# Kernel optimization log

Hardware: AMD Instinct MI355X
Metric: run time of the kernel (lower is better)

The kernel has to match this reference:

```python
import jax, jax.numpy as jnp
import numpy as np

N_NODES = 50000
N_EDGES = 800000
IN_CH = 128
HID = 128
OUT_CH = 10
N_GRAPHS = 64
BN_EPS = 1e-5


def _lin_init(k, fan_in, fan_out):
    k1, k2 = jax.random.split(k)
    s = 1.0 / np.sqrt(fan_in)
    W = jax.random.uniform(k1, (fan_in, fan_out), minval=-s, maxval=s, dtype=jnp.float32)
    b = jax.random.uniform(k2, (fan_out,), minval=-s, maxval=s, dtype=jnp.float32)
    return W, b


def setup_inputs() -> dict:
    key = jax.random.key(0)
    ks = jax.random.split(key, 12)
    x = jax.random.normal(ks[0], (N_NODES, IN_CH), dtype=jnp.float32)
    edge_index = jax.random.randint(ks[1], (2, N_EDGES), 0, N_NODES, dtype=jnp.int32)
    batch = jnp.sort(jax.random.randint(ks[2], (N_NODES,), 0, N_GRAPHS, dtype=jnp.int32))
    Wb0, bb0 = _lin_init(ks[3], IN_CH, HID)
    Wb1, bb1 = _lin_init(ks[4], HID, HID)
    Wa0, ba0 = _lin_init(ks[5], HID, HID)
    Wa1, ba1 = _lin_init(ks[6], HID, HID)
    Wa2, ba2 = _lin_init(ks[7], HID, HID)
    Wh0, bh0 = _lin_init(ks[8], HID, HID)
    Wh1, bh1 = _lin_init(ks[9], HID, HID)
    Wh2, bh2 = _lin_init(ks[10], HID, OUT_CH)
    ones = jnp.ones((HID,), jnp.float32)
    zeros = jnp.zeros((HID,), jnp.float32)
    return {
        'x': x, 'edge_index': edge_index, 'batch': batch, 'num_graphs': N_GRAPHS,
        'Wb0': Wb0, 'bb0': bb0, 'gb0': ones, 'betab0': zeros, 'Wb1': Wb1, 'bb1': bb1,
        'Wa0': Wa0, 'ba0': ba0, 'ga0': ones, 'bea0': zeros,
        'Wa1': Wa1, 'ba1': ba1, 'ga1': ones, 'bea1': zeros,
        'Wa2': Wa2, 'ba2': ba2,
        'Wh0': Wh0, 'bh0': bh0, 'Wh1': Wh1, 'bh1': bh1, 'Wh2': Wh2, 'bh2': bh2,
    }


def _gcn_edges(edge_index, n):
    # add self-loops, symmetric deg^{-1/2} normalization (PyG GCNConv default)
    loop = jnp.arange(n, dtype=edge_index.dtype)
    src = jnp.concatenate([edge_index[0], loop])
    dst = jnp.concatenate([edge_index[1], loop])
    deg = jax.ops.segment_sum(jnp.ones_like(dst, dtype=jnp.float32), dst, num_segments=n)
    dinv = jnp.where(deg > 0, jax.lax.rsqrt(deg), 0.0)
    return src, dst, dinv[src] * dinv[dst]


def _conv(h, W, b, src, dst, ew, n):
    hw = h @ W  # [N, F_out]
    agg = jax.ops.segment_sum(hw[src] * ew[:, None], dst, num_segments=n)
    return agg + b


def _bn(h, g, b):
    # BatchNorm1d with track_running_stats=False -> always batch statistics
    mean = jnp.mean(h, axis=0)
    var = jnp.var(h, axis=0)
    return g * (h - mean) * jax.lax.rsqrt(var + BN_EPS) + b


def _gelu(h):
    return jax.nn.gelu(h, approximate=False)


def reference(x, edge_index, batch, num_graphs,
              Wb0, bb0, gb0, betab0, Wb1, bb1,
              Wa0, ba0, ga0, bea0, Wa1, ba1, ga1, bea1, Wa2, ba2,
              Wh0, bh0, Wh1, bh1, Wh2, bh2):
    n = x.shape[0]
    src, dst, ew = _gcn_edges(edge_index, n)
    # GCN stack before (2 layers): conv -> bn -> gelu -> conv
    h = _conv(x, Wb0, bb0, src, dst, ew, n)
    h = _gelu(_bn(h, gb0, betab0))
    h = _conv(h, Wb1, bb1, src, dst, ew, n)
    # GCN stack after (3 layers)
    h = _conv(h, Wa0, ba0, src, dst, ew, n)
    h = _gelu(_bn(h, ga0, bea0))
    h = _conv(h, Wa1, ba1, src, dst, ew, n)
    h = _gelu(_bn(h, ga1, bea1))
    h = _conv(h, Wa2, ba2, src, dst, ew, n)
    # global mean pool per graph
    sums = jax.ops.segment_sum(h, batch, num_segments=num_graphs)
    cnt = jax.ops.segment_sum(jnp.ones((n,), jnp.float32), batch, num_segments=num_graphs)
    pooled = sums / jnp.maximum(cnt, 1.0)[:, None]
    # MLP head (dropout is identity in eval)
    y = _gelu(pooled @ Wh0 + bh0)
    y = _gelu(y @ Wh1 + bh1)
    return y @ Wh2 + bh2
```

## Files before the change

kernel.cpp:

```cpp
#include <hip/hip_runtime.h>
#include <math.h>

#define NN 50000
#define NE 800000
#define CH 128
#define NG 64
#define BN_EPS 1e-5f
#define POOL_CHUNK 64
#define BKT_SHIFT 9
#define NBKT ((NN + 511) >> 9)
#define PTILE 2048
#define NPART ((NE + PTILE - 1) / PTILE)
#define CAP 16384

typedef short bfrag8 __attribute__((ext_vector_type(8)));
typedef float facc4 __attribute__((ext_vector_type(4)));

__device__ __forceinline__ float gelu_f(float x) {
    return 0.5f * x * (1.0f + erff(x * 0.70710678118654752440f));
}

__device__ __forceinline__ unsigned int f2bf(float f) {
    unsigned int u = __float_as_uint(f);
    return (u + 0x7FFFu + ((u >> 16) & 1u)) >> 16;
}
__device__ __forceinline__ unsigned int pack_bf2(float lo, float hi) {
    return (f2bf(hi) << 16) | f2bf(lo);
}
__device__ __forceinline__ float bf_lo(unsigned int v) { return __uint_as_float(v << 16); }
__device__ __forceinline__ float bf_hi(unsigned int v) { return __uint_as_float(v & 0xFFFF0000u); }

__global__ __launch_bounds__(256) void part_k(const int* __restrict__ ei,
                                              int* __restrict__ btail,
                                              unsigned int* __restrict__ part,
                                              const float* __restrict__ W0,
                                              const float* __restrict__ W1,
                                              const float* __restrict__ W2,
                                              const float* __restrict__ W3,
                                              const float* __restrict__ W4,
                                              unsigned short* __restrict__ wf) {
    int t = threadIdx.x;
    if (blockIdx.x >= NPART) {
        int wb = blockIdx.x - NPART;
        int which = wb >> 3;
        int u = (wb & 7) * 256 + t;
        const float* W = (which == 0) ? W0 : (which == 1) ? W1 : (which == 2) ? W2
                       : (which == 3) ? W3 : W4;
        unsigned short* dst_wf = wf + (size_t)which * 16384;
        int nt = u >> 8, kc = (u >> 6) & 3, l = u & 63;
        int kbase = kc * 32 + (l >> 4) * 8;
        int n = nt * 16 + (l & 15);
        unsigned int p[4];
        #pragma unroll
        for (int jj = 0; jj < 4; ++jj) {
            float a = W[(kbase + 2 * jj) * 128 + n];
            float b = W[(kbase + 2 * jj + 1) * 128 + n];
            p[jj] = pack_bf2(a, b);
        }
        *(uint4*)(dst_wf + (size_t)u * 8) = make_uint4(p[0], p[1], p[2], p[3]);
        return;
    }

    __shared__ int lh[NBKT];
    __shared__ int gbase[NBKT];
    int base = blockIdx.x * PTILE;
    if (t < NBKT) lh[t] = 0;
    __syncthreads();
    int s[8], d[8], rk[8];
    #pragma unroll
    for (int i = 0; i < 8; ++i) {
        int e = base + i * 256 + t;
        if (e < NE) {
            s[i] = ei[e];
            d[i] = ei[NE + e];
            rk[i] = atomicAdd(&lh[d[i] >> BKT_SHIFT], 1);
        }
    }
    __syncthreads();
    if (t < NBKT && lh[t]) gbase[t] = t * CAP + atomicAdd(&btail[t], lh[t]);
    __syncthreads();
    #pragma unroll
    for (int i = 0; i < 8; ++i) {
        int e = base + i * 256 + t;
        if (e < NE) {
            int b = d[i] >> BKT_SHIFT;
            unsigned int ld = (unsigned int)(d[i] & 511);
            part[gbase[b] + rk[i]] = (ld << 16) | (unsigned int)s[i];
        }
    }
}

__global__ __launch_bounds__(256) void cscat2_k(const unsigned int* __restrict__ part,
                                                const int* __restrict__ btail,
                                                int* __restrict__ row_ptr,
                                                int* __restrict__ row_cnt,
                                                float* __restrict__ dinv,
                                                int* __restrict__ csr_src) {
    __shared__ int cnt_l[512];
    __shared__ int off_l[512];
    __shared__ int psc[256];
    int b = blockIdx.x;
    int n0 = b << BKT_SHIFT;
    int t = threadIdx.x;
    cnt_l[t] = 0;
    cnt_l[t + 256] = 0;
    __syncthreads();
    int e0 = b * CAP, e1 = e0 + btail[b];
    for (int e = e0 + t; e < e1; e += 256) {
        int ld = (int)(part[e] >> 16);
        atomicAdd(&cnt_l[ld], 1);
    }
    __syncthreads();
    int c0 = cnt_l[2 * t], c1 = cnt_l[2 * t + 1];
    psc[t] = c0 + c1;
    __syncthreads();
    for (int off = 1; off < 256; off <<= 1) {
        int a = (t >= off) ? psc[t - off] : 0;
        __syncthreads();
        psc[t] += a;
        __syncthreads();
    }
    int excl = (t == 0) ? 0 : psc[t - 1];
    off_l[2 * t] = excl;
    off_l[2 * t + 1] = excl + c0;
    #pragma unroll
    for (int k = 0; k < 2; ++k) {
        int ln = 2 * t + k;
        int n = n0 + ln;
        if (n < NN) {
            int c = (k == 0) ? c0 : c1;
            row_ptr[n] = e0 + off_l[ln];
            row_cnt[n] = c;
            dinv[n] = rsqrtf((float)c + 1.0f);
        }
    }
    __syncthreads();
    cnt_l[t] = 0;
    cnt_l[t + 256] = 0;
    __syncthreads();
    for (int e = e0 + t; e < e1; e += 256) {
        unsigned int p = part[e];
        int s = (int)(p & 0xFFFFu);
        int ld = (int)(p >> 16);
        int pos = e0 + off_l[ld] + atomicAdd(&cnt_l[ld], 1);
        csr_src[pos] = s;
    }
}

__device__ __forceinline__ void gemm_core(unsigned short* Alds, unsigned short* Wlds,
                                          const unsigned short* wfrag,
                                          const float* __restrict__ dinv, int tid,
                                          int row0, unsigned int* out16) {
    const int w = tid >> 6;
    const int l = tid & 63;
    const int quad = l >> 4;
    const int m = l & 15;

    float dv[4];
    #pragma unroll
    for (int r = 0; r < 4; ++r) {
        int row = row0 + w * 16 + quad * 4 + r;
        dv[r] = (row < NN) ? dinv[row] : 0.f;
    }

    #pragma unroll
    for (int i = 0; i < 8; ++i) {
        int linear = tid + i * 256;
        ((uint4*)Wlds)[linear] = ((const uint4*)wfrag)[linear];
    }
    __syncthreads();

    facc4 acc[8];
    #pragma unroll
    for (int nt = 0; nt < 8; ++nt) acc[nt] = (facc4){0.f, 0.f, 0.f, 0.f};

    #pragma unroll
    for (int kc = 0; kc < 4; ++kc) {
        bfrag8 a = *((const bfrag8*)(Alds + ((size_t)((w * 4 + kc) * 64 + l)) * 8));
        #pragma unroll
        for (int nt = 0; nt < 8; ++nt) {
            bfrag8 b = *((const bfrag8*)(Wlds + ((size_t)((nt * 4 + kc) * 64 + l)) * 8));
            acc[nt] = __builtin_amdgcn_mfma_f32_16x16x32_bf16(a, b, acc[nt], 0, 0, 0);
        }
    }

    #pragma unroll
    for (int nt = 0; nt < 8; ++nt) {
        #pragma unroll
        for (int r = 0; r < 4; ++r) {
            int row = row0 + w * 16 + quad * 4 + r;
            if (row < NN)
                ((unsigned short*)out16)[(size_t)row * 128 + nt * 16 + m] =
                    (unsigned short)f2bf(acc[nt][r] * dv[r]);
        }
    }
}

__global__ __launch_bounds__(256) void gemm_f32_k(const float* __restrict__ A,
                                                  const unsigned short* __restrict__ wfrag,
                                                  const float* __restrict__ dinv,
                                                  unsigned int* __restrict__ out16) {
    __shared__ unsigned short Alds[8192];
    __shared__ unsigned short Wlds[16384];
    const int tid = threadIdx.x;
    const int row0 = blockIdx.x * 64;
    #pragma unroll
    for (int i = 0; i < 4; ++i) {
        int linear = tid + i * 256;
        int r = linear >> 4;
        int g = linear & 15;
        float4 v0 = make_float4(0.f, 0.f, 0.f, 0.f);
        float4 v1 = make_float4(0.f, 0.f, 0.f, 0.f);
        if (row0 + r < NN) {
            const float4* src = (const float4*)&A[(size_t)(row0 + r) * 128 + g * 8];
            v0 = src[0];
            v1 = src[1];
        }
        int unit = (((r >> 4) * 4 + (g >> 2)) * 64) + ((g & 3) * 16) + (r & 15);
        *(uint4*)(Alds + (size_t)unit * 8) =
            make_uint4(pack_bf2(v0.x, v0.y), pack_bf2(v0.z, v0.w),
                       pack_bf2(v1.x, v1.y), pack_bf2(v1.z, v1.w));
    }
    gemm_core(Alds, Wlds, wfrag, dinv, tid, row0, out16);
}

__global__ __launch_bounds__(256) void gemm_bf16_k(const unsigned int* __restrict__ h16,
                                                   const unsigned short* __restrict__ wfrag,
                                                   const float* __restrict__ ss,
                                                   const float* __restrict__ dinv,
                                                   unsigned int* __restrict__ out16) {
    __shared__ unsigned short Alds[8192];
    __shared__ unsigned short Wlds[16384];
    const int tid = threadIdx.x;
    const int row0 = blockIdx.x * 64;
    #pragma unroll
    for (int i = 0; i < 4; ++i) {
        int linear = tid + i * 256;
        int r = linear >> 4;
        int g = linear & 15;
        uint4 v = make_uint4(0u, 0u, 0u, 0u);
        if (row0 + r < NN)
            v = ((const uint4*)h16)[(size_t)(row0 + r) * 16 + g];
        if (ss) {
            float4 sc0 = ((const float4*)ss)[g * 2];
            float4 sh0 = ((const float4*)ss)[32 + g * 2];
            float4 sc1 = ((const float4*)ss)[g * 2 + 1];
            float4 sh1 = ((const float4*)ss)[32 + g * 2 + 1];
            float f0 = gelu_f(bf_lo(v.x) * sc0.x + sh0.x);
            float f1 = gelu_f(bf_hi(v.x) * sc0.y + sh0.y);
            float f2 = gelu_f(bf_lo(v.y) * sc0.z + sh0.z);
            float f3 = gelu_f(bf_hi(v.y) * sc0.w + sh0.w);
            float f4 = gelu_f(bf_lo(v.z) * sc1.x + sh1.x);
            float f5 = gelu_f(bf_hi(v.z) * sc1.y + sh1.y);
            float f6 = gelu_f(bf_lo(v.w) * sc1.z + sh1.z);
            float f7 = gelu_f(bf_hi(v.w) * sc1.w + sh1.w);
            v = make_uint4(pack_bf2(f0, f1), pack_bf2(f2, f3),
                           pack_bf2(f4, f5), pack_bf2(f6, f7));
        }
        int unit = (((r >> 4) * 4 + (g >> 2)) * 64) + ((g & 3) * 16) + (r & 15);
        *(uint4*)(Alds + (size_t)unit * 8) = v;
    }
    gemm_core(Alds, Wlds, wfrag, dinv, tid, row0, out16);
}

__global__ __launch_bounds__(256) void csr_agg_k(const int* __restrict__ row_ptr,
                                                 const int* __restrict__ row_cnt,
                                                 const int* __restrict__ csr_src,
                                                 const unsigned int* __restrict__ hw16,
                                                 const float* __restrict__ bias,
                                                 const float* __restrict__ dinv,
                                                 unsigned int* __restrict__ out16,
                                                 float* __restrict__ stats) {
    int node = (blockIdx.x * 256 + threadIdx.x) >> 6;
    int lane = threadIdx.x & 63;
    float ox = 0.f, oy = 0.f;

    if (node < NN) {
        float di = dinv[node];
        float2 b = ((const float2*)bias)[lane];
        unsigned int hs = hw16[(size_t)node * 64 + lane];
        float a0x = bf_lo(hs), a0y = bf_hi(hs);
        float a1x = 0.f, a1y = 0.f;
        float a2x = 0.f, a2y = 0.f;
        float a3x = 0.f, a3y = 0.f;

        int j = row_ptr[node];
        int j1 = j + row_cnt[node];
        for (; j + 15 < j1; j += 16) {
            int s[16];
            #pragma unroll
            for (int k = 0; k < 16; ++k) s[k] = csr_src[j + k];
            unsigned int v[16];
            #pragma unroll
            for (int k = 0; k < 16; ++k) v[k] = hw16[(size_t)s[k] * 64 + lane];
            #pragma unroll
            for (int k = 0; k < 16; k += 8) {
                a0x += bf_lo(v[k + 0]) + bf_lo(v[k + 1]);
                a0y += bf_hi(v[k + 0]) + bf_hi(v[k + 1]);
                a1x += bf_lo(v[k + 2]) + bf_lo(v[k + 3]);
                a1y += bf_hi(v[k + 2]) + bf_hi(v[k + 3]);
                a2x += bf_lo(v[k + 4]) + bf_lo(v[k + 5]);
                a2y += bf_hi(v[k + 4]) + bf_hi(v[k + 5]);
                a3x += bf_lo(v[k + 6]) + bf_lo(v[k + 7]);
                a3y += bf_hi(v[k + 6]) + bf_hi(v[k + 7]);
            }
        }
        for (; j + 3 < j1; j += 4) {
            int s0 = csr_src[j], s1 = csr_src[j + 1];
            int s2 = csr_src[j + 2], s3 = csr_src[j + 3];
            unsigned int v0 = hw16[(size_t)s0 * 64 + lane];
            unsigned int v1 = hw16[(size_t)s1 * 64 + lane];
            unsigned int v2 = hw16[(size_t)s2 * 64 + lane];
            unsigned int v3 = hw16[(size_t)s3 * 64 + lane];
            a0x += bf_lo(v0) + bf_lo(v1);
            a0y += bf_hi(v0) + bf_hi(v1);
            a1x += bf_lo(v2) + bf_lo(v3);
            a1y += bf_hi(v2) + bf_hi(v3);
        }
        for (; j < j1; ++j) {
            int s = csr_src[j];
            unsigned int v = hw16[(size_t)s * 64 + lane];
            a0x += bf_lo(v);
            a0y += bf_hi(v);
        }
        ox = b.x + di * ((a0x + a1x) + (a2x + a3x));
        oy = b.y + di * ((a0y + a1y) + (a2y + a3y));
        out16[(size_t)node * 64 + lane] = pack_bf2(ox, oy);
    }

    if (stats) {
        __shared__ float red[1024];
        int t = threadIdx.x;
        red[t]       = ox;
        red[256 + t] = ox * ox;
        red[512 + t] = oy;
        red[768 + t] = oy * oy;
        __syncthreads();
        if (t < 64) {
            float tsx = red[t] + red[64 + t] + red[128 + t] + red[192 + t];
            float tqx = red[256 + t] + red[320 + t] + red[384 + t] + red[448 + t];
            float tsy = red[512 + t] + red[576 + t] + red[640 + t] + red[704 + t];
            float tqy = red[768 + t] + red[832 + t] + red[896 + t] + red[960 + t];
            float* dst = stats + (size_t)(blockIdx.x & 63) * 256;
            atomicAdd(&dst[2 * t], tsx);
            atomicAdd(&dst[2 * t + 1], tsy);
            atomicAdd(&dst[128 + 2 * t], tqx);
            atomicAdd(&dst[129 + 2 * t], tqy);
        }
    }
}

__global__ __launch_bounds__(128) void bn_fin_k(const float* __restrict__ stats,
                                                const float* __restrict__ g,
                                                const float* __restrict__ beta,
                                                float* __restrict__ ss) {
    int c = threadIdx.x;
    float sv = 0.f, qv = 0.f;
    #pragma unroll 8
    for (int i = 0; i < 64; ++i) {
        sv += stats[i * 256 + c];
        qv += stats[i * 256 + 128 + c];
    }
    float mean = sv * (1.0f / NN);
    float var = qv * (1.0f / NN) - mean * mean;
    float sc = g[c] * rsqrtf(var + BN_EPS);
    ss[c] = sc;
    ss[128 + c] = beta[c] - mean * sc;
}

__global__ __launch_bounds__(128) void pool_sum_k(const unsigned int* __restrict__ h16,
                                                  const int* __restrict__ batch,
                                                  float* __restrict__ sums) {
    int r0 = blockIdx.x * POOL_CHUNK;
    int r1 = min(r0 + POOL_CHUNK, NN);
    if (r0 >= NN) return;
    int c = threadIdx.x;
    int cp = c >> 1, hi = c & 1;
    float acc = 0.f;
    int g = batch[r0];
    for (int r = r0; r < r1; ++r) {
        int gr = batch[r];
        if (gr != g) {
            atomicAdd(&sums[g * 128 + c], acc);
            acc = 0.f;
            g = gr;
        }
        unsigned int v = h16[(size_t)r * 64 + cp];
        acc += hi ? bf_hi(v) : bf_lo(v);
    }
    atomicAdd(&sums[g * 128 + c], acc);
}

__device__ __forceinline__ int lower_bound_dev(const int* __restrict__ a, int n, int key) {
    int lo = 0, hi = n;
    while (lo < hi) {
        int mid = (lo + hi) >> 1;
        if (a[mid] < key) lo = mid + 1; else hi = mid;
    }
    return lo;
}

__global__ __launch_bounds__(128) void head_k(const float* __restrict__ psum,
                                              const int* __restrict__ batch,
                                              const float* __restrict__ W0, const float* __restrict__ b0,
                                              const float* __restrict__ W1, const float* __restrict__ b1,
                                              const float* __restrict__ W2, const float* __restrict__ b2,
                                              float* __restrict__ out) {
    __shared__ float r0[128], r1[128];
    int g = blockIdx.x, t = threadIdx.x;
    int a = lower_bound_dev(batch, NN, g);
    int b = lower_bound_dev(batch, NN, g + 1);
    float inv = 1.0f / fmaxf((float)(b - a), 1.0f);
    r0[t] = psum[g * 128 + t] * inv;
    __syncthreads();
    float acc = b0[t];
    for (int k = 0; k < 128; ++k) acc += r0[k] * W0[k * 128 + t];
    r1[t] = gelu_f(acc);
    __syncthreads();
    acc = b1[t];
    for (int k = 0; k < 128; ++k) acc += r1[k] * W1[k * 128 + t];
    float y = gelu_f(acc);
    __syncthreads();
    r0[t] = y;
    __syncthreads();
    if (t < 10) {
        acc = b2[t];
        for (int k = 0; k < 128; ++k) acc += r0[k] * W2[k * 10 + t];
        out[g * 10 + t] = acc;
    }
}

extern "C" void kernel_launch(void* const* d_in, const int* in_sizes, int n_in,
                              void* d_out, int out_size, void* d_ws, size_t ws_size,
                              hipStream_t stream) {
    const float* x      = (const float*)d_in[0];
    const int*   ei     = (const int*)d_in[1];
    const int*   batch  = (const int*)d_in[2];
    const float* Wb0    = (const float*)d_in[4];
    const float* bb0    = (const float*)d_in[5];
    const float* gb0    = (const float*)d_in[6];
    const float* betab0 = (const float*)d_in[7];
    const float* Wb1    = (const float*)d_in[8];
    const float* bb1    = (const float*)d_in[9];
    const float* Wa0    = (const float*)d_in[10];
    const float* ba0    = (const float*)d_in[11];
    const float* ga0    = (const float*)d_in[12];
    const float* bea0   = (const float*)d_in[13];
    const float* Wa1    = (const float*)d_in[14];
    const float* ba1    = (const float*)d_in[15];
    const float* ga1    = (const float*)d_in[16];
    const float* bea1   = (const float*)d_in[17];
    const float* Wa2    = (const float*)d_in[18];
    const float* ba2    = (const float*)d_in[19];
    const float* Wh0    = (const float*)d_in[20];
    const float* bh0    = (const float*)d_in[21];
    const float* Wh1    = (const float*)d_in[22];
    const float* bh1    = (const float*)d_in[23];
    const float* Wh2    = (const float*)d_in[24];
    const float* bh2    = (const float*)d_in[25];
    float* out = (float*)d_out;

    char* ws = (char*)d_ws;
    unsigned int* hw16 = (unsigned int*)ws;             ws += (size_t)NN * 64 * 4;
    unsigned int* hB   = (unsigned int*)ws;             ws += (size_t)NN * 64 * 4;
    unsigned int* hC   = (unsigned int*)ws;             ws += (size_t)NN * 64 * 4;
    float* dinv    = (float*)ws;                        ws += (size_t)NN * 4;
    int*   row_ptr = (int*)ws;                          ws += (size_t)(NN + 4) * 4;
    int*   row_cnt = (int*)ws;                          ws += (size_t)NN * 4;
    int*   csr_src = (int*)ws;                          ws += (size_t)NBKT * CAP * 4;
    unsigned int* part = (unsigned int*)ws;             ws += (size_t)NBKT * CAP * 4;
    unsigned short* wf = (unsigned short*)ws;           ws += (size_t)5 * 16384 * 2;
    float* ssbuf   = (float*)ws;                        ws += 256 * 4;
    char* zbase = ws;
    int*   btail   = (int*)ws;                          ws += 128 * 4;
    float* stats3  = (float*)ws;                        ws += (size_t)3 * 64 * 256 * 4;
    float* psum    = (float*)ws;                        ws += (size_t)NG * CH * 4;
    size_t zbytes = (size_t)(ws - zbase);

    unsigned short* wfb0 = wf;
    unsigned short* wfb1 = wf + 16384;
    unsigned short* wfa0 = wf + 2 * 16384;
    unsigned short* wfa1 = wf + 3 * 16384;
    unsigned short* wfa2 = wf + 4 * 16384;

    float* st0 = stats3;
    float* st1 = stats3 + 64 * 256;
    float* st2 = stats3 + 2 * 64 * 256;

    hipMemsetAsync(zbase, 0, zbytes, stream);

    part_k<<<NPART + 40, 256, 0, stream>>>(ei, btail, part, Wb0, Wb1, Wa0, Wa1, Wa2, wf);
    cscat2_k<<<NBKT, 256, 0, stream>>>(part, btail, row_ptr, row_cnt, dinv, csr_src);

    auto agg = [&](const float* b, unsigned int* o, float* stats) {
        csr_agg_k<<<(NN * 64 + 255) / 256, 256, 0, stream>>>(row_ptr, row_cnt, csr_src,
                                                             hw16, b, dinv, o, stats);
    };
    auto bn_fin = [&](const float* st, const float* g, const float* beta) {
        bn_fin_k<<<1, 128, 0, stream>>>(st, g, beta, ssbuf);
    };

    gemm_f32_k<<<(NN + 63) / 64, 256, 0, stream>>>(x, wfb0, dinv, hw16);
    agg(bb0, hB, st0);
    bn_fin(st0, gb0, betab0);
    gemm_bf16_k<<<(NN + 63) / 64, 256, 0, stream>>>(hB, wfb1, ssbuf, dinv, hw16);
    agg(bb1, hC, nullptr);
    gemm_bf16_k<<<(NN + 63) / 64, 256, 0, stream>>>(hC, wfa0, nullptr, dinv, hw16);
    agg(ba0, hB, st1);
    bn_fin(st1, ga0, bea0);
    gemm_bf16_k<<<(NN + 63) / 64, 256, 0, stream>>>(hB, wfa1, ssbuf, dinv, hw16);
    agg(ba1, hC, st2);
    bn_fin(st2, ga1, bea1);
    gemm_bf16_k<<<(NN + 63) / 64, 256, 0, stream>>>(hC, wfa2, ssbuf, dinv, hw16);
    agg(ba2, hB, nullptr);

    pool_sum_k<<<(NN + POOL_CHUNK - 1) / POOL_CHUNK, 128, 0, stream>>>(hB, batch, psum);
    head_k<<<NG, 128, 0, stream>>>(psum, batch, Wh0, bh0, Wh1, bh1, Wh2, bh2, out);
}
```

Before: 498.9 us.

## Split feature matrices into channel halves and aggregate each half in separate passes

Node feature buffers are stored as two 64-channel bf16 halves (128 bytes per row each). The aggregation kernel runs two passes, one per half, and each wavefront splits its edges between two 32-lane groups that are combined with a shuffle. The intent is to shrink the gather working set per pass so it fits in cache better, and to issue more independent edge loads per wave. In exchange, the kernel adds shuffles, doubles the index reads, and now depends on AGG_BLKS dividing NN exactly, since the bounds check was removed.

Measured after the change: 644.4 us. 29.2% more time.

```diff
diff --git a/kernel.cpp b/kernel.cpp
--- a/kernel.cpp
+++ b/kernel.cpp
@@ -12,6 +12,7 @@
 #define PTILE 2048
 #define NPART ((NE + PTILE - 1) / PTILE)
 #define CAP 16384
+#define AGG_BLKS (NN / 4)
 
 typedef short bfrag8 __attribute__((ext_vector_type(8)));
 typedef float facc4 __attribute__((ext_vector_type(4)));
@@ -150,7 +151,8 @@
 __device__ __forceinline__ void gemm_core(unsigned short* Alds, unsigned short* Wlds,
                                           const unsigned short* wfrag,
                                           const float* __restrict__ dinv, int tid,
-                                          int row0, unsigned int* out16) {
+                                          int row0,
+                                          unsigned int* out_lo, unsigned int* out_hi) {
     const int w = tid >> 6;
     const int l = tid & 63;
     const int quad = l >> 4;
@@ -186,12 +188,13 @@
 
     #pragma unroll
     for (int nt = 0; nt < 8; ++nt) {
+        unsigned short* So = (unsigned short*)((nt < 4) ? out_lo : out_hi);
+        int colh = (nt & 3) * 16 + m;
         #pragma unroll
         for (int r = 0; r < 4; ++r) {
             int row = row0 + w * 16 + quad * 4 + r;
             if (row < NN)
-                ((unsigned short*)out16)[(size_t)row * 128 + nt * 16 + m] =
-                    (unsigned short)f2bf(acc[nt][r] * dv[r]);
+                So[(size_t)row * 64 + colh] = (unsigned short)f2bf(acc[nt][r] * dv[r]);
         }
     }
 }
@@ -199,7 +202,8 @@
 __global__ __launch_bounds__(256) void gemm_f32_k(const float* __restrict__ A,
                                                   const unsigned short* __restrict__ wfrag,
                                                   const float* __restrict__ dinv,
-                                                  unsigned int* __restrict__ out16) {
+                                                  unsigned int* __restrict__ out_lo,
+                                                  unsigned int* __restrict__ out_hi) {
     __shared__ unsigned short Alds[8192];
     __shared__ unsigned short Wlds[16384];
     const int tid = threadIdx.x;
@@ -221,14 +225,16 @@
             make_uint4(pack_bf2(v0.x, v0.y), pack_bf2(v0.z, v0.w),
                        pack_bf2(v1.x, v1.y), pack_bf2(v1.z, v1.w));
     }
-    gemm_core(Alds, Wlds, wfrag, dinv, tid, row0, out16);
-}
-
-__global__ __launch_bounds__(256) void gemm_bf16_k(const unsigned int* __restrict__ h16,
+    gemm_core(Alds, Wlds, wfrag, dinv, tid, row0, out_lo, out_hi);
+}
+
+__global__ __launch_bounds__(256) void gemm_bf16_k(const unsigned int* __restrict__ h_lo,
+                                                   const unsigned int* __restrict__ h_hi,
                                                    const unsigned short* __restrict__ wfrag,
                                                    const float* __restrict__ ss,
                                                    const float* __restrict__ dinv,
-                                                   unsigned int* __restrict__ out16) {
+                                                   unsigned int* __restrict__ out_lo,
+                                                   unsigned int* __restrict__ out_hi) {
     __shared__ unsigned short Alds[8192];
     __shared__ unsigned short Wlds[16384];
     const int tid = threadIdx.x;
@@ -239,8 +245,10 @@
         int r = linear >> 4;
         int g = linear & 15;
         uint4 v = make_uint4(0u, 0u, 0u, 0u);
-        if (row0 + r < NN)
-            v = ((const uint4*)h16)[(size_t)(row0 + r) * 16 + g];
+        if (row0 + r < NN) {
+            v = (g < 8) ? ((const uint4*)h_lo)[(size_t)(row0 + r) * 8 + g]
+                        : ((const uint4*)h_hi)[(size_t)(row0 + r) * 8 + (g - 8)];
+        }
         if (ss) {
             float4 sc0 = ((const float4*)ss)[g * 2];
             float4 sh0 = ((const float4*)ss)[32 + g * 2];
@@ -260,92 +268,99 @@
         int unit = (((r >> 4) * 4 + (g >> 2)) * 64) + ((g & 3) * 16) + (r & 15);
         *(uint4*)(Alds + (size_t)unit * 8) = v;
     }
-    gemm_core(Alds, Wlds, wfrag, dinv, tid, row0, out16);
+    gemm_core(Alds, Wlds, wfrag, dinv, tid, row0, out_lo, out_hi);
 }
 
 __global__ __launch_bounds__(256) void csr_agg_k(const int* __restrict__ row_ptr,
                                                  const int* __restrict__ row_cnt,
                                                  const int* __restrict__ csr_src,
-                                                 const unsigned int* __restrict__ hw16,
+                                                 const unsigned int* __restrict__ Hlo,
+                                                 const unsigned int* __restrict__ Hhi,
                                                  const float* __restrict__ bias,
                                                  const float* __restrict__ dinv,
-                                                 unsigned int* __restrict__ out16,
+                                                 unsigned int* __restrict__ Olo,
+                                                 unsigned int* __restrict__ Ohi,
                                                  float* __restrict__ stats) {
-    int node = (blockIdx.x * 256 + threadIdx.x) >> 6;
+    int pass = (blockIdx.x >= AGG_BLKS) ? 1 : 0;
+    int blk = blockIdx.x - pass * AGG_BLKS;
+    const unsigned int* H = pass ? Hhi : Hlo;
+    unsigned int* O = pass ? Ohi : Olo;
+
+    int node = (blk * 256 + threadIdx.x) >> 6;
     int lane = threadIdx.x & 63;
+    int eh = lane >> 5;
+    int ch = lane & 31;
+
+    float a0x = 0.f, a0y = 0.f, a1x = 0.f, a1y = 0.f;
+    if (eh == 0) {
+        unsigned int hs = H[(size_t)node * 32 + ch];
+        a0x = bf_lo(hs);
+        a0y = bf_hi(hs);
+    }
+
+    int j = row_ptr[node];
+    int cnt = row_cnt[node];
+    int npairs = cnt >> 1;
+    for (; npairs >= 8; npairs -= 8, j += 16) {
+        int s[8];
+        #pragma unroll
+        for (int k = 0; k < 8; ++k) s[k] = csr_src[j + 2 * k + eh];
+        unsigned int v[8];
+        #pragma unroll
+        for (int k = 0; k < 8; ++k) v[k] = H[(size_t)s[k] * 32 + ch];
+        #pragma unroll
+        for (int k = 0; k < 8; k += 2) {
+            a0x += bf_lo(v[k]);     a0y += bf_hi(v[k]);
+            a1x += bf_lo(v[k + 1]); a1y += bf_hi(v[k + 1]);
+        }
+    }
+    for (; npairs > 0; --npairs, j += 2) {
+        int s = csr_src[j + eh];
+        unsigned int v = H[(size_t)s * 32 + ch];
+        a0x += bf_lo(v);
+        a0y += bf_hi(v);
+    }
+    if ((cnt & 1) && eh == 0) {
+        int s = csr_src[j];
+        unsigned int v = H[(size_t)s * 32 + ch];
+        a0x += bf_lo(v);
+        a0y += bf_hi(v);
+    }
+    float ax = a0x + a1x;
+    float ay = a0y + a1y;
+    ax += __shfl_down(ax, 32);
+    ay += __shfl_down(ay, 32);
+
     float ox = 0.f, oy = 0.f;
-
-    if (node < NN) {
+    if (eh == 0) {
         float di = dinv[node];
-        float2 b = ((const float2*)bias)[lane];
-        unsigned int hs = hw16[(size_t)node * 64 + lane];
-        float a0x = bf_lo(hs), a0y = bf_hi(hs);
-        float a1x = 0.f, a1y = 0.f;
-        float a2x = 0.f, a2y = 0.f;
-        float a3x = 0.f, a3y = 0.f;
-
-        int j = row_ptr[node];
-        int j1 = j + row_cnt[node];
-        for (; j + 15 < j1; j += 16) {
-            int s[16];
-            #pragma unroll
-            for (int k = 0; k < 16; ++k) s[k] = csr_src[j + k];
-            unsigned int v[16];
-            #pragma unroll
-            for (int k = 0; k < 16; ++k) v[k] = hw16[(size_t)s[k] * 64 + lane];
-            #pragma unroll
-            for (int k = 0; k < 16; k += 8) {
-                a0x += bf_lo(v[k + 0]) + bf_lo(v[k + 1]);
-                a0y += bf_hi(v[k + 0]) + bf_hi(v[k + 1]);
-                a1x += bf_lo(v[k + 2]) + bf_lo(v[k + 3]);
-                a1y += bf_hi(v[k + 2]) + bf_hi(v[k + 3]);
-                a2x += bf_lo(v[k + 4]) + bf_lo(v[k + 5]);
-                a2y += bf_hi(v[k + 4]) + bf_hi(v[k + 5]);
-                a3x += bf_lo(v[k + 6]) + bf_lo(v[k + 7]);
-                a3y += bf_hi(v[k + 6]) + bf_hi(v[k + 7]);
-            }
-        }
-        for (; j + 3 < j1; j += 4) {
-            int s0 = csr_src[j], s1 = csr_src[j + 1];
-            int s2 = csr_src[j + 2], s3 = csr_src[j + 3];
-            unsigned int v0 = hw16[(size_t)s0 * 64 + lane];
-            unsigned int v1 = hw16[(size_t)s1 * 64 + lane];
-            unsigned int v2 = hw16[(size_t)s2 * 64 + lane];
-            unsigned int v3 = hw16[(size_t)s3 * 64 + lane];
-            a0x += bf_lo(v0) + bf_lo(v1);
-            a0y += bf_hi(v0) + bf_hi(v1);
-            a1x += bf_lo(v2) + bf_lo(v3);
-            a1y += bf_hi(v2) + bf_hi(v3);
-        }
-        for (; j < j1; ++j) {
-            int s = csr_src[j];
-            unsigned int v = hw16[(size_t)s * 64 + lane];
-            a0x += bf_lo(v);
-            a0y += bf_hi(v);
-        }
-        ox = b.x + di * ((a0x + a1x) + (a2x + a3x));
-        oy = b.y + di * ((a0y + a1y) + (a2y + a3y));
-        out16[(size_t)node * 64 + lane] = pack_bf2(ox, oy);
+        float2 b = ((const float2*)bias)[pass * 32 + ch];
+        ox = b.x + di * ax;
+        oy = b.y + di * ay;
+        O[(size_t)node * 32 + ch] = pack_bf2(ox, oy);
     }
 
     if (stats) {
-        __shared__ float red[1024];
-        int t = threadIdx.x;
-        red[t]       = ox;
-        red[256 + t] = ox * ox;
-        red[512 + t] = oy;
-        red[768 + t] = oy * oy;
+        __shared__ float red[512];
+        int wv = threadIdx.x >> 6;
+        if (eh == 0) {
+            red[wv * 32 + ch]       = ox;
+            red[128 + wv * 32 + ch] = ox * ox;
+            red[256 + wv * 32 + ch] = oy;
+            red[384 + wv * 32 + ch] = oy * oy;
+        }
         __syncthreads();
-        if (t < 64) {
-            float tsx = red[t] + red[64 + t] + red[128 + t] + red[192 + t];
-            float tqx = red[256 + t] + red[320 + t] + red[384 + t] + red[448 + t];
-            float tsy = red[512 + t] + red[576 + t] + red[640 + t] + red[704 + t];
-            float tqy = red[768 + t] + red[832 + t] + red[896 + t] + red[960 + t];
-            float* dst = stats + (size_t)(blockIdx.x & 63) * 256;
-            atomicAdd(&dst[2 * t], tsx);
-            atomicAdd(&dst[2 * t + 1], tsy);
-            atomicAdd(&dst[128 + 2 * t], tqx);
-            atomicAdd(&dst[129 + 2 * t], tqy);
+        if (threadIdx.x < 32) {
+            int c = threadIdx.x;
+            float tsx = red[c] + red[32 + c] + red[64 + c] + red[96 + c];
+            float tqx = red[128 + c] + red[160 + c] + red[192 + c] + red[224 + c];
+            float tsy = red[256 + c] + red[288 + c] + red[320 + c] + red[352 + c];
+            float tqy = red[384 + c] + red[416 + c] + red[448 + c] + red[480 + c];
+            float* dstb = stats + (size_t)(blk & 63) * 256;
+            atomicAdd(&dstb[pass * 64 + 2 * c], tsx);
+            atomicAdd(&dstb[pass * 64 + 2 * c + 1], tsy);
+            atomicAdd(&dstb[128 + pass * 64 + 2 * c], tqx);
+            atomicAdd(&dstb[128 + pass * 64 + 2 * c + 1], tqy);
         }
     }
 }
@@ -368,7 +383,8 @@
     ss[128 + c] = beta[c] - mean * sc;
 }
 
-__global__ __launch_bounds__(128) void pool_sum_k(const unsigned int* __restrict__ h16,
+__global__ __launch_bounds__(128) void pool_sum_k(const unsigned int* __restrict__ h_lo,
+                                                  const unsigned int* __restrict__ h_hi,
                                                   const int* __restrict__ batch,
                                                   float* __restrict__ sums) {
     int r0 = blockIdx.x * POOL_CHUNK;
@@ -376,6 +392,8 @@
     if (r0 >= NN) return;
     int c = threadIdx.x;
     int cp = c >> 1, hi = c & 1;
+    const unsigned int* H = (cp < 32) ? h_lo : h_hi;
+    int cpl = cp & 31;
     float acc = 0.f;
     int g = batch[r0];
     for (int r = r0; r < r1; ++r) {
@@ -385,7 +403,7 @@
             acc = 0.f;
             g = gr;
         }
-        unsigned int v = h16[(size_t)r * 64 + cp];
+        unsigned int v = H[(size_t)r * 32 + cpl];
         acc += hi ? bf_hi(v) : bf_lo(v);
     }
     atomicAdd(&sums[g * 128 + c], acc);
@@ -461,9 +479,12 @@
     float* out = (float*)d_out;
 
     char* ws = (char*)d_ws;
-    unsigned int* hw16 = (unsigned int*)ws;             ws += (size_t)NN * 64 * 4;
-    unsigned int* hB   = (unsigned int*)ws;             ws += (size_t)NN * 64 * 4;
-    unsigned int* hC   = (unsigned int*)ws;             ws += (size_t)NN * 64 * 4;
+    unsigned int* hwLo = (unsigned int*)ws;             ws += (size_t)NN * 32 * 4;
+    unsigned int* hwHi = (unsigned int*)ws;             ws += (size_t)NN * 32 * 4;
+    unsigned int* hBlo = (unsigned int*)ws;             ws += (size_t)NN * 32 * 4;
+    unsigned int* hBhi = (unsigned int*)ws;             ws += (size_t)NN * 32 * 4;
+    unsigned int* hClo = (unsigned int*)ws;             ws += (size_t)NN * 32 * 4;
+    unsigned int* hChi = (unsigned int*)ws;             ws += (size_t)NN * 32 * 4;
     float* dinv    = (float*)ws;                        ws += (size_t)NN * 4;
     int*   row_ptr = (int*)ws;                          ws += (size_t)(NN + 4) * 4;
     int*   row_cnt = (int*)ws;                          ws += (size_t)NN * 4;
@@ -492,28 +513,28 @@
     part_k<<<NPART + 40, 256, 0, stream>>>(ei, btail, part, Wb0, Wb1, Wa0, Wa1, Wa2, wf);
     cscat2_k<<<NBKT, 256, 0, stream>>>(part, btail, row_ptr, row_cnt, dinv, csr_src);
 
-    auto agg = [&](const float* b, unsigned int* o, float* stats) {
-        csr_agg_k<<<(NN * 64 + 255) / 256, 256, 0, stream>>>(row_ptr, row_cnt, csr_src,
-                                                             hw16, b, dinv, o, stats);
+    auto agg = [&](const float* b, unsigned int* olo, unsigned int* ohi, float* stats) {
+        csr_agg_k<<<2 * AGG_BLKS, 256, 0, stream>>>(row_ptr, row_cnt, csr_src,
+                                                    hwLo, hwHi, b, dinv, olo, ohi, stats);
     };
     auto bn_fin = [&](const float* st, const float* g, const float* beta) {
         bn_fin_k<<<1, 128, 0, stream>>>(st, g, beta, ssbuf);
     };
 
-    gemm_f32_k<<<(NN + 63) / 64, 256, 0, stream>>>(x, wfb0, dinv, hw16);
-    agg(bb0, hB, st0);
+    gemm_f32_k<<<(NN + 63) / 64, 256, 0, stream>>>(x, wfb0, dinv, hwLo, hwHi);
+    agg(bb0, hBlo, hBhi, st0);
     bn_fin(st0, gb0, betab0);
-    gemm_bf16_k<<<(NN + 63) / 64, 256, 0, stream>>>(hB, wfb1, ssbuf, dinv, hw16);
-    agg(bb1, hC, nullptr);
-    gemm_bf16_k<<<(NN + 63) / 64, 256, 0, stream>>>(hC, wfa0, nullptr, dinv, hw16);
-    agg(ba0, hB, st1);
+    gemm_bf16_k<<<(NN + 63) / 64, 256, 0, stream>>>(hBlo, hBhi, wfb1, ssbuf, dinv, hwLo, hwHi);
+    agg(bb1, hClo, hChi, nullptr);
+    gemm_bf16_k<<<(NN + 63) / 64, 256, 0, stream>>>(hClo, hChi, wfa0, nullptr, dinv, hwLo, hwHi);
+    agg(ba0, hBlo, hBhi, st1);
     bn_fin(st1, ga0, bea0);
-    gemm_bf16_k<<<(NN + 63) / 64, 256, 0, stream>>>(hB, wfa1, ssbuf, dinv, hw16);
-    agg(ba1, hC, st2);
+    gemm_bf16_k<<<(NN + 63) / 64, 256, 0, stream>>>(hBlo, hBhi, wfa1, ssbuf, dinv, hwLo, hwHi);
+    agg(ba1, hClo, hChi, st2);
     bn_fin(st2, ga1, bea1);
-    gemm_bf16_k<<<(NN + 63) / 64, 256, 0, stream>>>(hC, wfa2, ssbuf, dinv, hw16);
-    agg(ba2, hB, nullptr);
-
-    pool_sum_k<<<(NN + POOL_CHUNK - 1) / POOL_CHUNK, 128, 0, stream>>>(hB, batch, psum);
+    gemm_bf16_k<<<(NN + 63) / 64, 256, 0, stream>>>(hClo, hChi, wfa2, ssbuf, dinv, hwLo, hwHi);
+    agg(ba2, hBlo, hBhi, nullptr);
+
+    pool_sum_k<<<(NN + POOL_CHUNK - 1) / POOL_CHUNK, 128, 0, stream>>>(hBlo, hBhi, batch, psum);
     head_k<<<NG, 128, 0, stream>>>(psum, batch, Wh0, bh0, Wh1, bh1, Wh2, bh2, out);
 }
```
